# Optimization experiments

Hardware: AMD Instinct MI355X
Metric: run time of the kernel (lower is better)

Reference implementation:

```python
import jax, jax.numpy as jnp
import numpy as np

EPS = 1e-5

def conv1x1(x, w, b):
    # x: [B,C,H,W], w: [O,C], b: [O]
    return jnp.einsum('bchw,oc->bohw', x, w) + b[None, :, None, None]

def batchnorm(z, gamma, beta):
    # training-mode BN over (N,H,W) as in SynchronizedBatchNorm2d forward
    m = jnp.mean(z, axis=(0, 2, 3), keepdims=True)
    v = jnp.var(z, axis=(0, 2, 3), keepdims=True)
    zn = (z - m) * jax.lax.rsqrt(v + EPS)
    return zn * gamma[None, :, None, None] + beta[None, :, None, None]

def setup_inputs() -> dict:
    key = jax.random.key(0)
    ks = jax.random.split(key, 12)
    B, C, H, W = 4, 512, 64, 64
    Ck, Cv = 256, 256
    s_in = 1.0 / np.sqrt(C)
    s_v = 1.0 / np.sqrt(Cv)
    return {
        'x': jax.random.normal(ks[0], (B, C, H, W), jnp.float32),
        'wq': jax.random.normal(ks[1], (Ck, C), jnp.float32) * s_in,
        'bq': jnp.zeros((Ck,), jnp.float32),
        'gq': jnp.ones((Ck,), jnp.float32),
        'betaq': jnp.zeros((Ck,), jnp.float32),
        'wk': jax.random.normal(ks[2], (Ck, C), jnp.float32) * s_in,
        'bk': jnp.zeros((Ck,), jnp.float32),
        'gk': jnp.ones((Ck,), jnp.float32),
        'betak': jnp.zeros((Ck,), jnp.float32),
        'wv': jax.random.normal(ks[3], (Cv, C), jnp.float32) * s_in,
        'bv': jnp.zeros((Cv,), jnp.float32),
        'wW': jax.random.normal(ks[4], (C, Cv), jnp.float32) * s_v,
        'bW': jnp.zeros((C,), jnp.float32),
    }

def reference(x, wq, bq, gq, betaq, wk, bk, gk, betak, wv, bv, wW, bW):
    B, C, H, W = x.shape
    Ck = wq.shape[0]
    Cv = wv.shape[0]
    N = H * W
    # f_query / f_key: conv1x1 -> BN -> ReLU
    q = jax.nn.relu(batchnorm(conv1x1(x, wq, bq), gq, betaq)).reshape(B, Ck, N)          # [B,Ck,N]
    k = jax.nn.relu(batchnorm(conv1x1(x, wk, bk), gk, betak)).reshape(B, Ck, N)          # [B,Ck,N]
    v = conv1x1(x, wv, bv).reshape(B, Cv, N)                                             # [B,Cv,N]
    # att_map = key^T @ query, scaled, softmax over last dim (query positions)
    att = jnp.einsum('bcn,bcm->bnm', k, q) * (Ck ** -0.5)                                # [B,N,N]
    att = jax.nn.softmax(att, axis=2)
    # context = att @ value^T -> [B,N,Cv] -> [B,Cv,H,W]
    ctx = jnp.einsum('bnm,bcm->bcn', att, v).reshape(B, Cv, H, W)
    out = conv1x1(ctx, wW, bW) + x
    return out
```

## Files before the change

kernel.cpp:

```cpp
#include <hip/hip_runtime.h>

typedef __attribute__((ext_vector_type(8))) __bf16 bfx8;
typedef __attribute__((ext_vector_type(4))) float f32x4;

__device__ __forceinline__ float s2f(unsigned short s) {
  return __uint_as_float((unsigned int)s << 16);
}
__device__ __forceinline__ unsigned short f2s(float f) {
  return (unsigned short)((__float_as_uint(f) + 0x8000u) >> 16);
}

template<int BM, int BN, int BK>
__device__ __forceinline__ void gemm_core_async(
    const unsigned short* __restrict__ Ag, int lda,
    const unsigned short* __restrict__ Bg, int ldb, int K,
    unsigned short* As, unsigned short* Bs, f32x4* acc)
{
  static_assert(BK == 64, "BK must be 64 (128B rows)");
  constexpr int WM = BM / 2, WN = BN / 2;
  constexpr int MT = WM / 16, NT = WN / 16;
  constexpr int SA = BM / 8, SB = BN / 8;
  const int tid = threadIdx.x;
  const int lane = tid & 63, wave = tid >> 6;
  const int lr = lane & 15, quad = lane >> 4;
  const int sw = lr & 7;
  const int rl = lane >> 3;
  const int vg = (lane & 7) ^ rl;
  const int wm = (wave >> 1) * WM, wn = (wave & 1) * WN;

  for (int k0 = 0; k0 < K; k0 += BK) {
#pragma unroll
    for (int s = wave; s < SA; s += 4) {
      const unsigned short* g = Ag + (size_t)(s * 8 + rl) * lda + k0 + vg * 8;
      __builtin_amdgcn_global_load_lds(
          (__attribute__((address_space(1))) void*)g,
          (__attribute__((address_space(3))) void*)(As + s * 512), 16, 0, 0);
    }
#pragma unroll
    for (int s = wave; s < SB; s += 4) {
      const unsigned short* g = Bg + (size_t)(s * 8 + rl) * ldb + k0 + vg * 8;
      __builtin_amdgcn_global_load_lds(
          (__attribute__((address_space(1))) void*)g,
          (__attribute__((address_space(3))) void*)(Bs + s * 512), 16, 0, 0);
    }
    __syncthreads();
#pragma unroll
    for (int kk = 0; kk < BK; kk += 32) {
      const int kv = kk >> 3;
      bfx8 af[MT], bfr[NT];
#pragma unroll
      for (int i = 0; i < MT; ++i)
        af[i] = *(const bfx8*)(As + (wm + i * 16 + lr) * BK
                               + (((quad + kv) ^ sw) << 3));
#pragma unroll
      for (int j = 0; j < NT; ++j)
        bfr[j] = *(const bfx8*)(Bs + (wn + j * 16 + lr) * BK
                                + (((quad + kv) ^ sw) << 3));
#pragma unroll
      for (int i = 0; i < MT; ++i)
#pragma unroll
        for (int j = 0; j < NT; ++j)
          acc[i * NT + j] = __builtin_amdgcn_mfma_f32_16x16x32_bf16(
              af[i], bfr[j], acc[i * NT + j], 0, 0, 0);
    }
    __syncthreads();
  }
}

__global__ __launch_bounds__(256) void k_pre(
    const float* __restrict__ x, unsigned short* __restrict__ xt,
    const float* __restrict__ wq, const float* __restrict__ wk,
    const float* __restrict__ wv, const float* __restrict__ wW,
    unsigned short* __restrict__ wqk, unsigned short* __restrict__ wvb,
    unsigned short* __restrict__ wWb)
{
  const int bid = blockIdx.x, tid = threadIdx.x;
  if (bid < 2048) {
    __shared__ float t[64][65];
    const int b = bid >> 9, c0 = ((bid >> 6) & 7) * 64, n0 = (bid & 63) * 64;
    const float* xb = x + ((size_t)b << 21);
    const int hi = tid >> 6, lo = tid & 63;
#pragma unroll
    for (int p = 0; p < 16; ++p)
      t[hi + p * 4][lo] = xb[(size_t)(c0 + hi + p * 4) * 4096 + n0 + lo];
    __syncthreads();
    unsigned short* xtb = xt + ((size_t)b << 21);
#pragma unroll
    for (int p = 0; p < 16; ++p)
      xtb[(size_t)(n0 + hi + p * 4) * 512 + c0 + lo] = f2s(t[lo][hi + p * 4]);
  } else {
    int i = (bid - 2048) * 256 + tid;
    wqk[i] = f2s(i < 131072 ? wq[i] : wk[i - 131072]);
    if (i < 131072) { wvb[i] = f2s(wv[i]); wWb[i] = f2s(wW[i]); }
  }
}

__global__ __launch_bounds__(256) void k_qkv(
    const unsigned short* __restrict__ xt, const unsigned short* __restrict__ wqk,
    const unsigned short* __restrict__ wvb, const float* __restrict__ bv,
    unsigned short* __restrict__ zt, unsigned short* __restrict__ v,
    float* __restrict__ stat)
{
  __shared__ __align__(16) unsigned short As[128 * 64], Bs[128 * 64];
  f32x4 acc[16] = {};
  const int b = blockIdx.z, n0 = blockIdx.x * 128, t = blockIdx.y;
  const int lane = threadIdx.x & 63, wave = threadIdx.x >> 6;
  const int lr = lane & 15, quad = lane >> 4;
  const int wm = (wave >> 1) * 64, wn = (wave & 1) * 64;

  if (t < 4) {
    const int o0 = t * 128;
    gemm_core_async<128, 128, 64>(xt + ((size_t)b * 4096 + n0) * 512, 512,
                                  wqk + (size_t)o0 * 512, 512, 512, As, Bs, acc);
    float s[4] = {}, ss[4] = {};
#pragma unroll
    for (int i = 0; i < 4; ++i)
#pragma unroll
      for (int j = 0; j < 4; ++j)
#pragma unroll
        for (int r = 0; r < 4; ++r) {
          float a = acc[i * 4 + j][r];
          int row = wm + i * 16 + quad * 4 + r, col = wn + j * 16 + lr;
          zt[((size_t)b * 4096 + n0 + row) * 512 + o0 + col] = f2s(a);
          s[j] += a; ss[j] += a * a;
        }
#pragma unroll
    for (int j = 0; j < 4; ++j) {
      s[j]  += __shfl_down(s[j], 32, 64);  s[j]  += __shfl_down(s[j], 16, 64);
      ss[j] += __shfl_down(ss[j], 32, 64); ss[j] += __shfl_down(ss[j], 16, 64);
      if (quad == 0) {
        int o = o0 + wn + j * 16 + lr;
        atomicAdd(&stat[o * 2], s[j]);
        atomicAdd(&stat[o * 2 + 1], ss[j]);
      }
    }
  } else {
    const int cv0 = (t - 4) * 128;
    gemm_core_async<128, 128, 64>(wvb + (size_t)cv0 * 512, 512,
                                  xt + ((size_t)b * 4096 + n0) * 512, 512, 512,
                                  As, Bs, acc);
#pragma unroll
    for (int i = 0; i < 4; ++i)
#pragma unroll
      for (int j = 0; j < 4; ++j)
#pragma unroll
        for (int r = 0; r < 4; ++r) {
          int row = wm + i * 16 + quad * 4 + r, col = wn + j * 16 + lr;
          v[((size_t)b * 256 + cv0 + row) * 4096 + n0 + col] =
              f2s(acc[i * 4 + j][r] + bv[cv0 + row]);
        }
  }
}

__global__ __launch_bounds__(256) void k_bnrelu(
    const unsigned short* __restrict__ zt, const float* __restrict__ stats_raw,
    const float* __restrict__ gq, const float* __restrict__ betaq,
    const float* __restrict__ gk, const float* __restrict__ betak,
    unsigned short* __restrict__ qt, unsigned short* __restrict__ kt)
{
  const int t = threadIdx.x;
  const float mA = stats_raw[t * 2] * (1.f / 16384.f);
  const float vA = stats_raw[t * 2 + 1] * (1.f / 16384.f) - mA * mA;
  const float scA = rsqrtf(vA + 1e-5f) * gq[t], beA = betaq[t];
  const float mB = stats_raw[(t + 256) * 2] * (1.f / 16384.f);
  const float vB = stats_raw[(t + 256) * 2 + 1] * (1.f / 16384.f) - mB * mB;
  const float scB = rsqrtf(vB + 1e-5f) * gk[t], beB = betak[t];
  const int r0 = blockIdx.x * 16;
  for (int r = r0; r < r0 + 16; ++r) {
    float a = s2f(zt[(size_t)r * 512 + t]);
    qt[(size_t)r * 256 + t] = f2s(fmaxf((a - mA) * scA + beA, 0.f));
    float c = s2f(zt[(size_t)r * 512 + t + 256]);
    kt[(size_t)r * 256 + t] = f2s(fmaxf((c - mB) * scB + beB, 0.f));
  }
}

__global__ __launch_bounds__(512, 2) void k_att(
    const unsigned short* __restrict__ qt, const unsigned short* __restrict__ kt,
    const unsigned short* __restrict__ v, float* __restrict__ opart,
    float* __restrict__ lsum)
{
  __shared__ __align__(16) unsigned short Ks[4 * 8192];
  __shared__ __align__(16) unsigned short BufA[2 * 8192];
  __shared__ __align__(16) unsigned short BufB[2 * 8192];
  __shared__ __align__(16) unsigned short Ps[2 * 8192];

  const int tid = threadIdx.x;
  const int lane = tid & 63, wave = tid >> 6;
  const int lr = lane & 15, quad = lane >> 4;
  const int sw = lr & 7;
  const int rl = lane >> 3;
  const int vg = (lane & 7) ^ rl;
  const int rn = wave >> 2, cw = wave & 3;

  const int ms = blockIdx.x, n0 = blockIdx.y * 128, b = blockIdx.z;

  const unsigned short* Qg = qt + (size_t)(b * 4096 + ms * 2048) * 256;
  const unsigned short* Vg = v + (size_t)(b * 256) * 4096 + ms * 2048;

  auto stageQ = [&](unsigned short* dst, int trow, int h) {
#pragma unroll
    for (int s = wave; s < 32; s += 8) {
      const unsigned short* g = Qg
          + (size_t)(trow * 128 + (s & 15) * 8 + rl) * 256
          + h * 128 + (s >> 4) * 64 + vg * 8;
      __builtin_amdgcn_global_load_lds(
          (__attribute__((address_space(1))) void*)g,
          (__attribute__((address_space(3))) void*)(dst + s * 512), 16, 0, 0);
    }
  };
  auto stageV = [&](unsigned short* dst, int trow, int ch) {
#pragma unroll
    for (int s = wave; s < 32; s += 8) {
      const unsigned short* g = Vg + (size_t)(s * 8 + rl) * 4096
                                + trow * 128 + ch * 64 + vg * 8;
      __builtin_amdgcn_global_load_lds(
          (__attribute__((address_space(1))) void*)g,
          (__attribute__((address_space(3))) void*)(dst + s * 512), 16, 0, 0);
    }
  };

  f32x4 oacc[16] = {};
  float rsum[16] = {};
  const float C1 = 0.0625f * 1.44269504f;
  const float C0 = -20.0f * 1.44269504f;

  {
    const unsigned short* Kg = kt + (size_t)(b * 4096 + n0) * 256;
#pragma unroll
    for (int s = wave; s < 64; s += 8) {
      const unsigned short* g = Kg + (size_t)((s & 15) * 8 + rl) * 256
                                + (s >> 4) * 64 + vg * 8;
      __builtin_amdgcn_global_load_lds(
          (__attribute__((address_space(1))) void*)g,
          (__attribute__((address_space(3))) void*)(Ks + s * 512), 16, 0, 0);
    }
  }
  stageQ(BufA, 0, 0);
  __syncthreads();

#pragma unroll 1
  for (int t = 0; t < 16; ++t) {
    f32x4 sacc[8] = {};

    auto computeS = [&](const unsigned short* Qb, int h) {
#pragma unroll
      for (int p2 = 0; p2 < 2; ++p2)
#pragma unroll
        for (int kk = 0; kk < 2; ++kk) {
          const int kv = kk * 4;
          bfx8 af[4], bq[2];
#pragma unroll
          for (int i = 0; i < 4; ++i)
            af[i] = *(const bfx8*)(Ks + (h * 2 + p2) * 8192
                     + (rn * 64 + i * 16 + lr) * 64 + (((quad + kv) ^ sw) << 3));
#pragma unroll
          for (int j = 0; j < 2; ++j)
            bq[j] = *(const bfx8*)(Qb + p2 * 8192
                     + (cw * 32 + j * 16 + lr) * 64 + (((quad + kv) ^ sw) << 3));
#pragma unroll
          for (int i = 0; i < 4; ++i)
#pragma unroll
            for (int j = 0; j < 2; ++j)
              sacc[i * 2 + j] = __builtin_amdgcn_mfma_f32_16x16x32_bf16(
                  af[i], bq[j], sacc[i * 2 + j], 0, 0, 0);
        }
    };
    auto computeO = [&](const unsigned short* Vb, int ch) {
#pragma unroll
      for (int kk = 0; kk < 2; ++kk) {
        const int kv = kk * 4;
        bfx8 ap[4], bvf[4];
#pragma unroll
        for (int i = 0; i < 4; ++i)
          ap[i] = *(const bfx8*)(Ps + ch * 8192
                   + (rn * 64 + i * 16 + lr) * 64 + (((quad + kv) ^ sw) << 3));
#pragma unroll
        for (int j = 0; j < 4; ++j)
          bvf[j] = *(const bfx8*)(Vb
                   + (cw * 64 + j * 16 + lr) * 64 + (((quad + kv) ^ sw) << 3));
#pragma unroll
        for (int i = 0; i < 4; ++i)
#pragma unroll
          for (int j = 0; j < 4; ++j)
            oacc[i * 4 + j] = __builtin_amdgcn_mfma_f32_16x16x32_bf16(
                ap[i], bvf[j], oacc[i * 4 + j], 0, 0, 0);
      }
    };

    stageQ(BufB, t, 1);
    computeS(BufA, 0);
    __syncthreads();

    stageV(BufA, t, 0);
    computeS(BufB, 1);
#pragma unroll
    for (int i = 0; i < 4; ++i)
#pragma unroll
      for (int j = 0; j < 2; ++j)
#pragma unroll
        for (int r = 0; r < 4; ++r) {
          float p = __builtin_amdgcn_exp2f(fmaf(sacc[i * 2 + j][r], C1, C0));
          rsum[i * 4 + r] += p;
          const int row = rn * 64 + i * 16 + quad * 4 + r;
          const int cvec = cw * 4 + j * 2 + (lr >> 3);
          Ps[(cvec >> 3) * 8192 + row * 64
             + (((cvec & 7) ^ (row & 7)) << 3) + (lr & 7)] = f2s(p);
        }
    __syncthreads();

    stageV(BufB, t, 1);
    computeO(BufA, 0);
    __syncthreads();

    if (t < 15) stageQ(BufA, t + 1, 0);
    computeO(BufB, 1);
    __syncthreads();
  }

  float* op = opart + ((size_t)(ms * 4 + b) * 4096 + n0) * 256;
#pragma unroll
  for (int i = 0; i < 4; ++i)
#pragma unroll
    for (int j = 0; j < 4; ++j)
#pragma unroll
      for (int r = 0; r < 4; ++r) {
        const int row = rn * 64 + i * 16 + quad * 4 + r;
        const int col = cw * 64 + j * 16 + lr;
        op[(size_t)row * 256 + col] = oacc[i * 4 + j][r];
      }
  float* l = lsum + b * 4096 + n0;
#pragma unroll
  for (int i = 0; i < 4; ++i)
#pragma unroll
    for (int r = 0; r < 4; ++r) {
      float rs = rsum[i * 4 + r];
      rs += __shfl_down(rs, 8, 16);
      rs += __shfl_down(rs, 4, 16);
      rs += __shfl_down(rs, 2, 16);
      rs += __shfl_down(rs, 1, 16);
      if (lr == 0) atomicAdd(&l[rn * 64 + i * 16 + quad * 4 + r], rs);
    }
}

__global__ __launch_bounds__(256) void k_red(
    const float* __restrict__ opart, const float* __restrict__ lsum,
    unsigned short* __restrict__ ctx)
{
  const int g = blockIdx.x, c = threadIdx.x;
  const float s = opart[(size_t)g * 256 + c]
                + opart[((size_t)g + 16384) * 256 + c];
  ctx[(size_t)g * 256 + c] = f2s(s / lsum[g]);
}

__global__ __launch_bounds__(256) void k_out(
    const unsigned short* __restrict__ wWb, const float* __restrict__ bW,
    const unsigned short* __restrict__ ctx, const float* __restrict__ x,
    float* __restrict__ out)
{
  __shared__ __align__(16) unsigned short As[128 * 64], Bs[128 * 64];
  f32x4 acc[16] = {};
  const int b = blockIdx.z, n0 = blockIdx.x * 128, o0 = blockIdx.y * 128;
  gemm_core_async<128, 128, 64>(wWb + (size_t)o0 * 256, 256,
                                ctx + ((size_t)b * 4096 + n0) * 256, 256, 256,
                                As, Bs, acc);
  const int lane = threadIdx.x & 63, wave = threadIdx.x >> 6;
  const int lr = lane & 15, quad = lane >> 4;
  const int wm = (wave >> 1) * 64, wn = (wave & 1) * 64;
#pragma unroll
  for (int i = 0; i < 4; ++i)
#pragma unroll
    for (int j = 0; j < 4; ++j)
#pragma unroll
      for (int r = 0; r < 4; ++r) {
        int row = wm + i * 16 + quad * 4 + r, col = wn + j * 16 + lr;
        size_t idx = ((size_t)b * 512 + o0 + row) * 4096 + n0 + col;
        out[idx] = acc[i * 4 + j][r] + bW[o0 + row] + x[idx];
      }
}

extern "C" void kernel_launch(void* const* d_in, const int* in_sizes, int n_in,
                              void* d_out, int out_size, void* d_ws, size_t ws_size,
                              hipStream_t stream)
{
  const float* x     = (const float*)d_in[0];
  const float* wq    = (const float*)d_in[1];
  const float* gq    = (const float*)d_in[3];
  const float* betaq = (const float*)d_in[4];
  const float* wk    = (const float*)d_in[5];
  const float* gk    = (const float*)d_in[7];
  const float* betak = (const float*)d_in[8];
  const float* wv    = (const float*)d_in[9];
  const float* bv    = (const float*)d_in[10];
  const float* wW    = (const float*)d_in[11];
  const float* bW    = (const float*)d_in[12];
  float* out = (float*)d_out;

  char* ws = (char*)d_ws;
  unsigned short* qt   = (unsigned short*)(ws);
  unsigned short* kt   = (unsigned short*)(ws + 8388608);
  unsigned short* v    = (unsigned short*)(ws + 16777216);
  unsigned short* ctx  = (unsigned short*)(ws + 25165824);
  unsigned short* wqk  = (unsigned short*)(ws + 33554432);
  unsigned short* wvb  = (unsigned short*)(ws + 34078720);
  unsigned short* wWb  = (unsigned short*)(ws + 34340864);
  float*          stat = (float*)         (ws + 34603008);
  float*          lsum = (float*)         (ws + 34607104);
  float*          opart= (float*)         (ws + 35651584);
  unsigned short* xt   = (unsigned short*)(ws + 35651584);
  unsigned short* zt   = (unsigned short*)(ws + 52428800);

  (void)hipMemsetAsync(stat, 0, 69632, stream);
  k_pre   <<<3072, 256, 0, stream>>>(x, xt, wq, wk, wv, wW, wqk, wvb, wWb);
  k_qkv   <<<dim3(32, 6, 4), 256, 0, stream>>>(xt, wqk, wvb, bv, zt, v, stat);
  k_bnrelu<<<1024, 256, 0, stream>>>(zt, stat, gq, betaq, gk, betak, qt, kt);
  k_att   <<<dim3(2, 32, 4), 512, 0, stream>>>(qt, kt, v, opart, lsum);
  k_red   <<<16384, 256, 0, stream>>>(opart, lsum, ctx);
  k_out   <<<dim3(32, 4, 4), 256, 0, stream>>>(wWb, bW, ctx, x, out);
}
```

Measured before the change: 246.5 us.

## Load V fragments directly to registers and cache first K half in registers

After: 403.3 us. 1.64x slower.

```diff
diff --git a/kernel.cpp b/kernel.cpp
--- a/kernel.cpp
+++ b/kernel.cpp
@@ -192,7 +192,8 @@
   const int vg = (lane & 7) ^ rl;
   const int rn = wave >> 2, cw = wave & 3;
 
-  const int ms = blockIdx.x, n0 = blockIdx.y * 128, b = blockIdx.z;
+  const int ms = blockIdx.x & 1, b = blockIdx.x >> 1;
+  const int n0 = blockIdx.y * 128;
 
   const unsigned short* Qg = qt + (size_t)(b * 4096 + ms * 2048) * 256;
   const unsigned short* Vg = v + (size_t)(b * 256) * 4096 + ms * 2048;
@@ -208,15 +209,14 @@
           (__attribute__((address_space(3))) void*)(dst + s * 512), 16, 0, 0);
     }
   };
-  auto stageV = [&](unsigned short* dst, int trow, int ch) {
-#pragma unroll
-    for (int s = wave; s < 32; s += 8) {
-      const unsigned short* g = Vg + (size_t)(s * 8 + rl) * 4096
-                                + trow * 128 + ch * 64 + vg * 8;
-      __builtin_amdgcn_global_load_lds(
-          (__attribute__((address_space(1))) void*)g,
-          (__attribute__((address_space(3))) void*)(dst + s * 512), 16, 0, 0);
-    }
+  auto loadV = [&](bfx8 (&vf)[2][4], int trow, int ch) {
+#pragma unroll
+    for (int kk = 0; kk < 2; ++kk)
+#pragma unroll
+      for (int j = 0; j < 4; ++j)
+        vf[kk][j] = *(const bfx8*)(Vg
+            + (size_t)(cw * 64 + j * 16 + lr) * 4096
+            + trow * 128 + ch * 64 + kk * 32 + quad * 8);
   };
 
   f32x4 oacc[16] = {};
@@ -238,61 +238,82 @@
   stageQ(BufA, 0, 0);
   __syncthreads();
 
+  bfx8 kfrag[16];
+#pragma unroll
+  for (int i = 0; i < 4; ++i)
+#pragma unroll
+    for (int p2 = 0; p2 < 2; ++p2)
+#pragma unroll
+      for (int kk = 0; kk < 2; ++kk)
+        kfrag[(i * 2 + p2) * 2 + kk] = *(const bfx8*)(Ks + p2 * 8192
+            + (rn * 64 + i * 16 + lr) * 64 + (((quad + kk * 4) ^ sw) << 3));
+
 #pragma unroll 1
   for (int t = 0; t < 16; ++t) {
     f32x4 sacc[8] = {};
-
-    auto computeS = [&](const unsigned short* Qb, int h) {
-#pragma unroll
-      for (int p2 = 0; p2 < 2; ++p2)
-#pragma unroll
-        for (int kk = 0; kk < 2; ++kk) {
-          const int kv = kk * 4;
-          bfx8 af[4], bq[2];
-#pragma unroll
-          for (int i = 0; i < 4; ++i)
-            af[i] = *(const bfx8*)(Ks + (h * 2 + p2) * 8192
-                     + (rn * 64 + i * 16 + lr) * 64 + (((quad + kv) ^ sw) << 3));
-#pragma unroll
-          for (int j = 0; j < 2; ++j)
-            bq[j] = *(const bfx8*)(Qb + p2 * 8192
-                     + (cw * 32 + j * 16 + lr) * 64 + (((quad + kv) ^ sw) << 3));
-#pragma unroll
-          for (int i = 0; i < 4; ++i)
-#pragma unroll
-            for (int j = 0; j < 2; ++j)
-              sacc[i * 2 + j] = __builtin_amdgcn_mfma_f32_16x16x32_bf16(
-                  af[i], bq[j], sacc[i * 2 + j], 0, 0, 0);
-        }
-    };
-    auto computeO = [&](const unsigned short* Vb, int ch) {
+    bfx8 vf0[2][4], vf1[2][4];
+
+    auto computeO = [&](const bfx8 (&vf)[2][4], int ch) {
 #pragma unroll
       for (int kk = 0; kk < 2; ++kk) {
         const int kv = kk * 4;
-        bfx8 ap[4], bvf[4];
+        bfx8 ap[4];
 #pragma unroll
         for (int i = 0; i < 4; ++i)
           ap[i] = *(const bfx8*)(Ps + ch * 8192
                    + (rn * 64 + i * 16 + lr) * 64 + (((quad + kv) ^ sw) << 3));
 #pragma unroll
-        for (int j = 0; j < 4; ++j)
-          bvf[j] = *(const bfx8*)(Vb
-                   + (cw * 64 + j * 16 + lr) * 64 + (((quad + kv) ^ sw) << 3));
-#pragma unroll
         for (int i = 0; i < 4; ++i)
 #pragma unroll
           for (int j = 0; j < 4; ++j)
             oacc[i * 4 + j] = __builtin_amdgcn_mfma_f32_16x16x32_bf16(
-                ap[i], bvf[j], oacc[i * 4 + j], 0, 0, 0);
+                ap[i], vf[kk][j], oacc[i * 4 + j], 0, 0, 0);
       }
     };
 
+    loadV(vf0, t, 0);
     stageQ(BufB, t, 1);
-    computeS(BufA, 0);
-    __syncthreads();
-
-    stageV(BufA, t, 0);
-    computeS(BufB, 1);
+#pragma unroll
+    for (int p2 = 0; p2 < 2; ++p2)
+#pragma unroll
+      for (int kk = 0; kk < 2; ++kk) {
+        const int kv = kk * 4;
+        bfx8 bq[2];
+#pragma unroll
+        for (int j = 0; j < 2; ++j)
+          bq[j] = *(const bfx8*)(BufA + p2 * 8192
+                   + (cw * 32 + j * 16 + lr) * 64 + (((quad + kv) ^ sw) << 3));
+#pragma unroll
+        for (int i = 0; i < 4; ++i)
+#pragma unroll
+          for (int j = 0; j < 2; ++j)
+            sacc[i * 2 + j] = __builtin_amdgcn_mfma_f32_16x16x32_bf16(
+                kfrag[(i * 2 + p2) * 2 + kk], bq[j], sacc[i * 2 + j], 0, 0, 0);
+      }
+    __syncthreads();
+
+    if (t < 15) stageQ(BufA, t + 1, 0);
+#pragma unroll
+    for (int p2 = 0; p2 < 2; ++p2)
+#pragma unroll
+      for (int kk = 0; kk < 2; ++kk) {
+        const int kv = kk * 4;
+        bfx8 af[4], bq[2];
+#pragma unroll
+        for (int i = 0; i < 4; ++i)
+          af[i] = *(const bfx8*)(Ks + (2 + p2) * 8192
+                   + (rn * 64 + i * 16 + lr) * 64 + (((quad + kv) ^ sw) << 3));
+#pragma unroll
+        for (int j = 0; j < 2; ++j)
+          bq[j] = *(const bfx8*)(BufB + p2 * 8192
+                   + (cw * 32 + j * 16 + lr) * 64 + (((quad + kv) ^ sw) << 3));
+#pragma unroll
+        for (int i = 0; i < 4; ++i)
+#pragma unroll
+          for (int j = 0; j < 2; ++j)
+            sacc[i * 2 + j] = __builtin_amdgcn_mfma_f32_16x16x32_bf16(
+                af[i], bq[j], sacc[i * 2 + j], 0, 0, 0);
+      }
 #pragma unroll
     for (int i = 0; i < 4; ++i)
 #pragma unroll
@@ -308,12 +329,10 @@
         }
     __syncthreads();
 
-    stageV(BufB, t, 1);
-    computeO(BufA, 0);
-    __syncthreads();
-
-    if (t < 15) stageQ(BufA, t + 1, 0);
-    computeO(BufB, 1);
+    loadV(vf1, t, 1);
+    computeO(vf0, 0);
+
+    computeO(vf1, 1);
     __syncthreads();
   }
 
@@ -413,7 +432,7 @@
   k_pre   <<<3072, 256, 0, stream>>>(x, xt, wq, wk, wv, wW, wqk, wvb, wWb);
   k_qkv   <<<dim3(32, 6, 4), 256, 0, stream>>>(xt, wqk, wvb, bv, zt, v, stat);
   k_bnrelu<<<1024, 256, 0, stream>>>(zt, stat, gq, betaq, gk, betak, qt, kt);
-  k_att   <<<dim3(2, 32, 4), 512, 0, stream>>>(qt, kt, v, opart, lsum);
+  k_att   <<<dim3(8, 32), 512, 0, stream>>>(qt, kt, v, opart, lsum);
   k_red   <<<16384, 256, 0, stream>>>(opart, lsum, ctx);
   k_out   <<<dim3(32, 4, 4), 256, 0, stream>>>(wWb, bW, ctx, x, out);
 }
```
